# Performance work log

Measured on AMD Instinct MI355X. Metric: run time of the kernel, lower is better.

The kernel has to match this reference:

```python
import jax, jax.numpy as jnp
import numpy as np

N = 50000
E = 800000
IN_DIM = 128
HID = 128
OUT = 128
HEADS = 4
HD_HID = HID // HEADS   # 32
HD_OUT = OUT // HEADS   # 32
NEG_SLOPE = 0.2


def gat_layer(H, src, dst, W, a_src, a_dst, b, num_nodes):
    """Standard GAT layer with concatenated heads.
    H: [N, Fin]; W: [Fin, heads*hd]; a_src/a_dst: [heads, hd]; b: [heads*hd]."""
    heads, hd = a_src.shape
    h = (H @ W).reshape(num_nodes, heads, hd)            # [N, H, D]
    alpha_s = jnp.einsum('nhd,hd->nh', h, a_src)         # [N, H]
    alpha_d = jnp.einsum('nhd,hd->nh', h, a_dst)         # [N, H]
    logits = alpha_s[src] + alpha_d[dst]                 # [E, H]
    logits = jax.nn.leaky_relu(logits, NEG_SLOPE)
    # segment softmax over incoming edges of each destination node
    seg_max = jax.ops.segment_max(logits, dst, num_segments=num_nodes)
    seg_max = jnp.where(jnp.isfinite(seg_max), seg_max, 0.0)
    ex = jnp.exp(logits - seg_max[dst])                  # [E, H]
    denom = jax.ops.segment_sum(ex, dst, num_segments=num_nodes)  # [N, H]
    att = ex / jnp.maximum(denom, 1e-16)[dst]            # [E, H]
    msg = att[:, :, None] * h[src]                       # [E, H, D]
    out = jax.ops.segment_sum(msg, dst, num_segments=num_nodes)   # [N, H, D]
    return out.reshape(num_nodes, heads * hd) + b


def setup_inputs() -> dict:
    key = jax.random.key(0)
    ks = jax.random.split(key, 10)
    X_all = jax.random.normal(ks[0], (N, IN_DIM), dtype=jnp.float32)
    edge_index = jax.random.randint(ks[1], (2, E), 0, N, dtype=jnp.int64)
    s0 = 1.0 / np.sqrt(IN_DIM)
    s1 = 1.0 / np.sqrt(HID)
    W0 = jax.random.normal(ks[2], (IN_DIM, HEADS * HD_HID), dtype=jnp.float32) * s0
    a_src0 = jax.random.normal(ks[3], (HEADS, HD_HID), dtype=jnp.float32) * s1
    a_dst0 = jax.random.normal(ks[4], (HEADS, HD_HID), dtype=jnp.float32) * s1
    b0 = jnp.zeros((HEADS * HD_HID,), dtype=jnp.float32)
    W1 = jax.random.normal(ks[5], (HID, HEADS * HD_OUT), dtype=jnp.float32) * s1
    a_src1 = jax.random.normal(ks[6], (HEADS, HD_OUT), dtype=jnp.float32) * s1
    a_dst1 = jax.random.normal(ks[7], (HEADS, HD_OUT), dtype=jnp.float32) * s1
    b1 = jnp.zeros((HEADS * HD_OUT,), dtype=jnp.float32)
    return {"X_all": X_all, "edge_index": edge_index,
            "W0": W0, "a_src0": a_src0, "a_dst0": a_dst0, "b0": b0,
            "W1": W1, "a_src1": a_src1, "a_dst1": a_dst1, "b1": b1}


def reference(X_all, edge_index, W0, a_src0, a_dst0, b0, W1, a_src1, a_dst1, b1):
    src, dst = edge_index[0], edge_index[1]
    num_nodes = X_all.shape[0]
    # layer 1 + ELU (dropout is identity in eval mode)
    H = gat_layer(X_all, src, dst, W0, a_src0, a_dst0, b0, num_nodes)
    H = jax.nn.elu(H)
    # layer 2 + ELU
    H = gat_layer(H, src, dst, W1, a_src1, a_dst1, b1, num_nodes)
    H = jax.nn.elu(H)
    return H
```

## Files before the change

kernel.cpp:

```cpp
#include <hip/hip_runtime.h>
#include <math.h>
#include <float.h>

#define NNODES 50000
#define NEDGES 800000

#define KB    196
#define NPB   256
#define CAPB  4608
#define EPB   4096
#define NABLK ((NEDGES + EPB - 1) / EPB)

typedef __attribute__((ext_vector_type(4))) _Float16 half4;
typedef __attribute__((ext_vector_type(8))) _Float16 half8;
typedef __attribute__((ext_vector_type(4))) float f32x4;

__global__ __launch_bounds__(256) void bininit_kernel(int* __restrict__ bincur) {
    int t = threadIdx.x;
    if (t < KB) bincur[t] = t * CAPB;
}

__global__ __launch_bounds__(256) void binA_kernel(
    const int* __restrict__ src, const int* __restrict__ dst,
    int* __restrict__ bincur, unsigned* __restrict__ binned)
{
    __shared__ int lhist[KB];
    __shared__ int lstart[KB];
    __shared__ int lcur[KB];
    __shared__ int gbase[KB];
    __shared__ unsigned lbuf[EPB];
    __shared__ int wtot[4];

    int t = threadIdx.x;
    int e0 = blockIdx.x * EPB;
    int ecnt = NEDGES - e0; if (ecnt > EPB) ecnt = EPB;

    for (int b = t; b < KB; b += 256) lhist[b] = 0;
    __syncthreads();

    for (int idx = t; idx < ecnt; idx += 256)
        atomicAdd(&lhist[((unsigned)dst[e0 + idx]) >> 8], 1);
    __syncthreads();

    {
        int lane = t & 63, w = t >> 6;
        int v = (t < KB) ? lhist[t] : 0;
        int x = v;
#pragma unroll
        for (int off = 1; off < 64; off <<= 1) {
            int y = __shfl_up(x, off, 64);
            if (lane >= off) x += y;
        }
        if (lane == 63) wtot[w] = x;
        __syncthreads();
        int wpre = 0;
#pragma unroll
        for (int j = 0; j < 4; ++j) if (j < w) wpre += wtot[j];
        int ex = wpre + x - v;
        if (t < KB) { lstart[t] = ex; lcur[t] = ex; }
    }
    __syncthreads();

    if (t < KB) {
        int c = lhist[t];
        gbase[t] = c ? atomicAdd(&bincur[t], c) : 0;
    }
    __syncthreads();

    for (int idx = t; idx < ecnt; idx += 256) {
        unsigned d = (unsigned)dst[e0 + idx];
        unsigned s = (unsigned)src[e0 + idx];
        int pos = atomicAdd(&lcur[d >> 8], 1);
        lbuf[pos] = (d << 16) | s;
    }
    __syncthreads();

    for (int idx = t; idx < ecnt; idx += 256) {
        unsigned p = lbuf[idx];
        int b = p >> 24;
        binned[gbase[b] + (idx - lstart[b])] = p;
    }
}

__global__ __launch_bounds__(256) void binB_kernel(
    const unsigned* __restrict__ binned, const int* __restrict__ bincur,
    int* __restrict__ csr_src, int2* __restrict__ node_info)
{
    __shared__ int lhist[NPB];
    __shared__ int lcur[NPB];
    __shared__ int wtot[4];
    int k = blockIdx.x;
    int t = threadIdx.x;
    int base = k * CAPB;
    int cnt = bincur[k] - base;

    lhist[t] = 0;
    __syncthreads();

    for (int i = t; i < cnt; i += 256)
        atomicAdd(&lhist[(binned[base + i] >> 16) & 0xFF], 1);
    __syncthreads();

    int lane = t & 63, w = t >> 6;
    int v = lhist[t];
    int x = v;
#pragma unroll
    for (int off = 1; off < 64; off <<= 1) {
        int y = __shfl_up(x, off, 64);
        if (lane >= off) x += y;
    }
    if (lane == 63) wtot[w] = x;
    __syncthreads();
    int wpre = 0;
#pragma unroll
    for (int j = 0; j < 4; ++j) if (j < w) wpre += wtot[j];
    int ex = wpre + x - v;
    lcur[t] = ex;
    int node = k * NPB + t;
    if (node < NNODES) node_info[node] = make_int2(base + ex, v);
    __syncthreads();

    for (int i = t; i < cnt; i += 256) {
        unsigned p = binned[base + i];
        int ln = (p >> 16) & 0xFF;
        int pos = atomicAdd(&lcur[ln], 1);
        csr_src[base + pos] = (int)(p & 0xFFFFu);
    }
}

__global__ __launch_bounds__(256) void prep_kernel(
    const float* __restrict__ X, const float* __restrict__ W0,
    const float* __restrict__ W1, _Float16* __restrict__ X16,
    _Float16* __restrict__ W0t, _Float16* __restrict__ W1t)
{
    int i = blockIdx.x * 256 + threadIdx.x;
    int stride = gridDim.x * 256;
    const int nx4 = NNODES * 128 / 4;
    for (int idx = i; idx < nx4; idx += stride) {
        float4 v = ((const float4*)X)[idx];
        half4 h = {(_Float16)v.x, (_Float16)v.y, (_Float16)v.z, (_Float16)v.w};
        ((half4*)X16)[idx] = h;
    }
    for (int idx = i; idx < 128 * 128; idx += stride) {
        int cc = idx >> 7, k = idx & 127;
        W0t[idx] = (_Float16)W0[k * 128 + cc];
        W1t[idx] = (_Float16)W1[k * 128 + cc];
    }
}

#define GP 136
__global__ __launch_bounds__(256) void gemm_mfma_kernel(
    const _Float16* __restrict__ A, const _Float16* __restrict__ Wt,
    const float* __restrict__ avs, const float* __restrict__ avd,
    _Float16* __restrict__ Hh, float* __restrict__ alpha_s,
    float* __restrict__ alpha_d, int nrows)
{
    __shared__ _Float16 Xs[64 * GP];
    __shared__ _Float16 Ws[128 * GP];

    int t = threadIdx.x;
    int brow = blockIdx.x * 64;

    {
        int r = t >> 2, q = t & 3;
        int grow = brow + r;
        half8 v0 = {}, v1 = {}, v2 = {}, v3 = {};
        if (grow < nrows) {
            const half8* p = (const half8*)(A + (size_t)grow * 128 + q * 32);
            v0 = p[0]; v1 = p[1]; v2 = p[2]; v3 = p[3];
        }
        _Float16* d = Xs + r * GP + q * 32;
        *(half8*)(d + 0)  = v0; *(half8*)(d + 8)  = v1;
        *(half8*)(d + 16) = v2; *(half8*)(d + 24) = v3;
    }
    {
        int wr = t >> 1, wh = t & 1;
        const half8* p = (const half8*)(Wt + wr * 128 + wh * 64);
        _Float16* d = Ws + wr * GP + wh * 64;
#pragma unroll
        for (int j = 0; j < 8; ++j) *(half8*)(d + j * 8) = p[j];
    }
    __syncthreads();

    int wv = t >> 6, l = t & 63;
    int lrow = l & 15;
    int lk8  = (l >> 4) * 8;

    f32x4 acc[8];
#pragma unroll
    for (int n = 0; n < 8; ++n) acc[n] = (f32x4){0.f, 0.f, 0.f, 0.f};

    const _Float16* xbase = Xs + (wv * 16 + lrow) * GP + lk8;
#pragma unroll
    for (int kk = 0; kk < 4; ++kk) {
        half8 a = *(const half8*)(xbase + kk * 32);
#pragma unroll
        for (int n = 0; n < 8; ++n) {
            half8 bf = *(const half8*)(Ws + (n * 16 + lrow) * GP + kk * 32 + lk8);
            acc[n] = __builtin_amdgcn_mfma_f32_16x16x32_f16(a, bf, acc[n], 0, 0, 0);
        }
    }

    int c = lrow;
    int g = l >> 4;
#pragma unroll
    for (int n = 0; n < 8; ++n) {
#pragma unroll
        for (int r = 0; r < 4; ++r) {
            int row = brow + wv * 16 + g * 4 + r;
            if (row < nrows)
                Hh[(size_t)row * 128 + n * 16 + c] = (_Float16)acc[n][r];
        }
    }
#pragma unroll
    for (int hd = 0; hd < 4; ++hd) {
        float as0 = avs[hd * 32 + c], as1 = avs[hd * 32 + 16 + c];
        float ad0 = avd[hd * 32 + c], ad1 = avd[hd * 32 + 16 + c];
#pragma unroll
        for (int r = 0; r < 4; ++r) {
            float ps = acc[2 * hd][r] * as0 + acc[2 * hd + 1][r] * as1;
            float pd = acc[2 * hd][r] * ad0 + acc[2 * hd + 1][r] * ad1;
            ps += __shfl_xor(ps, 1); ps += __shfl_xor(ps, 2);
            ps += __shfl_xor(ps, 4); ps += __shfl_xor(ps, 8);
            pd += __shfl_xor(pd, 1); pd += __shfl_xor(pd, 2);
            pd += __shfl_xor(pd, 4); pd += __shfl_xor(pd, 8);
            if (c == 0) {
                int row = brow + wv * 16 + g * 4 + r;
                if (row < nrows) {
                    alpha_s[row * 4 + hd] = ps;
                    alpha_d[row * 4 + hd] = pd;
                }
            }
        }
    }
}

template <bool F16OUT>
__global__ __launch_bounds__(256) void att_gather_kernel(
    const int* __restrict__ csr_src, const int2* __restrict__ node_info,
    const float* __restrict__ alpha_s, const float* __restrict__ alpha_d,
    const _Float16* __restrict__ hbuf, const float* __restrict__ b,
    float* __restrict__ out32, _Float16* __restrict__ out16)
{
    int node = blockIdx.x * 4 + (threadIdx.x >> 6);
    if (node >= NNODES) return;
    int lane = threadIdx.x & 63;
    int half = lane >> 5;
    int q    = lane & 31;
    int f    = q * 4;
    int hh   = q >> 3;
    int2 bi = node_info[node];
    int beg = bi.x, end = bi.x + bi.y;
    float ad = alpha_d[node * 4 + hh];

    float4 a4 = make_float4(0.f, 0.f, 0.f, 0.f);
    float den = 0.f;
    int i = beg + half;
    for (; i + 6 < end; i += 8) {
        int s0 = csr_src[i];
        int s1 = csr_src[i + 2];
        int s2 = csr_src[i + 4];
        int s3 = csr_src[i + 6];
        float l0 = alpha_s[s0 * 4 + hh] + ad;
        float l1 = alpha_s[s1 * 4 + hh] + ad;
        float l2 = alpha_s[s2 * 4 + hh] + ad;
        float l3 = alpha_s[s3 * 4 + hh] + ad;
        half4 h0 = *(const half4*)(hbuf + (size_t)s0 * 128 + f);
        half4 h1 = *(const half4*)(hbuf + (size_t)s1 * 128 + f);
        half4 h2 = *(const half4*)(hbuf + (size_t)s2 * 128 + f);
        half4 h3 = *(const half4*)(hbuf + (size_t)s3 * 128 + f);
        l0 = (l0 >= 0.f) ? l0 : 0.2f * l0;
        l1 = (l1 >= 0.f) ? l1 : 0.2f * l1;
        l2 = (l2 >= 0.f) ? l2 : 0.2f * l2;
        l3 = (l3 >= 0.f) ? l3 : 0.2f * l3;
        float e0 = __expf(l0);
        float e1 = __expf(l1);
        float e2 = __expf(l2);
        float e3 = __expf(l3);
        den += (e0 + e1) + (e2 + e3);
        a4.x = fmaf(e0, (float)h0[0], a4.x); a4.y = fmaf(e0, (float)h0[1], a4.y);
        a4.z = fmaf(e0, (float)h0[2], a4.z); a4.w = fmaf(e0, (float)h0[3], a4.w);
        a4.x = fmaf(e1, (float)h1[0], a4.x); a4.y = fmaf(e1, (float)h1[1], a4.y);
        a4.z = fmaf(e1, (float)h1[2], a4.z); a4.w = fmaf(e1, (float)h1[3], a4.w);
        a4.x = fmaf(e2, (float)h2[0], a4.x); a4.y = fmaf(e2, (float)h2[1], a4.y);
        a4.z = fmaf(e2, (float)h2[2], a4.z); a4.w = fmaf(e2, (float)h2[3], a4.w);
        a4.x = fmaf(e3, (float)h3[0], a4.x); a4.y = fmaf(e3, (float)h3[1], a4.y);
        a4.z = fmaf(e3, (float)h3[2], a4.z); a4.w = fmaf(e3, (float)h3[3], a4.w);
    }
    for (; i < end; i += 2) {
        int s0 = csr_src[i];
        float l0 = alpha_s[s0 * 4 + hh] + ad;
        l0 = (l0 >= 0.f) ? l0 : 0.2f * l0;
        float e0 = __expf(l0);
        half4 h0 = *(const half4*)(hbuf + (size_t)s0 * 128 + f);
        den += e0;
        a4.x = fmaf(e0, (float)h0[0], a4.x); a4.y = fmaf(e0, (float)h0[1], a4.y);
        a4.z = fmaf(e0, (float)h0[2], a4.z); a4.w = fmaf(e0, (float)h0[3], a4.w);
    }

    a4.x += __shfl_xor(a4.x, 32);
    a4.y += __shfl_xor(a4.y, 32);
    a4.z += __shfl_xor(a4.z, 32);
    a4.w += __shfl_xor(a4.w, 32);
    den  += __shfl_xor(den, 32);

    if (half == 0) {
        float rd = 1.f / fmaxf(den, 1e-16f);
        float4 bv = *(const float4*)(b + f);
        float x0 = a4.x * rd + bv.x;
        float x1 = a4.y * rd + bv.y;
        float x2 = a4.z * rd + bv.z;
        float x3 = a4.w * rd + bv.w;
        x0 = (x0 > 0.f) ? x0 : expm1f(x0);
        x1 = (x1 > 0.f) ? x1 : expm1f(x1);
        x2 = (x2 > 0.f) ? x2 : expm1f(x2);
        x3 = (x3 > 0.f) ? x3 : expm1f(x3);
        if (F16OUT) {
            half4 hv = {(_Float16)x0, (_Float16)x1, (_Float16)x2, (_Float16)x3};
            *(half4*)(out16 + (size_t)node * 128 + f) = hv;
        } else {
            *(float4*)(out32 + (size_t)node * 128 + f) = make_float4(x0, x1, x2, x3);
        }
    }
}

extern "C" void kernel_launch(void* const* d_in, const int* in_sizes, int n_in,
                              void* d_out, int out_size, void* d_ws, size_t ws_size,
                              hipStream_t stream) {
    const float* X    = (const float*)d_in[0];
    const int*   ei   = (const int*)d_in[1];
    const float* W0   = (const float*)d_in[2];
    const float* as0  = (const float*)d_in[3];
    const float* ad0  = (const float*)d_in[4];
    const float* b0   = (const float*)d_in[5];
    const float* W1   = (const float*)d_in[6];
    const float* as1  = (const float*)d_in[7];
    const float* ad1  = (const float*)d_in[8];
    const float* b1   = (const float*)d_in[9];

    const int* srcp = ei;
    const int* dstp = ei + NEDGES;

    _Float16* X16  = (_Float16*)d_ws;
    _Float16* h16  = X16 + 6400000;
    _Float16* ho16 = h16 + 6400000;
    _Float16* W0t  = ho16 + 6400000;
    _Float16* W1t  = W0t + 16384;
    float* as_ = (float*)(W1t + 16384);
    float* ad_ = as_ + 200000;
    unsigned* binned = (unsigned*)(ad_ + 200000);
    int*  csr_src   = (int*)(binned + (KB + 1) * CAPB);
    int2* node_info = (int2*)(csr_src + KB * CAPB);
    int*  bincur    = (int*)(node_info + NNODES);

    bininit_kernel<<<1, 256, 0, stream>>>(bincur);
    binA_kernel<<<NABLK, 256, 0, stream>>>(srcp, dstp, bincur, binned);
    binB_kernel<<<KB, 256, 0, stream>>>(binned, bincur, csr_src, node_info);

    prep_kernel<<<2048, 256, 0, stream>>>(X, W0, W1, X16, W0t, W1t);

    const int NODE_BLOCKS = (NNODES + 3) / 4;
    const int GEMM_BLOCKS = (NNODES + 63) / 64;

    gemm_mfma_kernel<<<GEMM_BLOCKS, 256, 0, stream>>>(
        X16, W0t, as0, ad0, h16, as_, ad_, NNODES);
    att_gather_kernel<true><<<NODE_BLOCKS, 256, 0, stream>>>(
        csr_src, node_info, as_, ad_, h16, b0, nullptr, ho16);

    gemm_mfma_kernel<<<GEMM_BLOCKS, 256, 0, stream>>>(
        ho16, W1t, as1, ad1, h16, as_, ad_, NNODES);
    att_gather_kernel<false><<<NODE_BLOCKS, 256, 0, stream>>>(
        csr_src, node_info, as_, ad_, h16, b1, (float*)d_out, nullptr);
}
```

Baseline: 160.2 us.

## Fuse fp32-to-fp16 input conversion into GEMM and widen gather to half8 lanes

The separate X-to-fp16 conversion pass is removed. The first GEMM now reads fp32 X directly and converts it while staging into shared memory, which saves a full write and re-read of a 12.8 MB fp16 copy. The attention gather is reorganised so each node's wave has 16 lanes each covering 8 features with half8 loads, and 4 edge groups run in parallel, reduced with two shuffles. This raises edge-level parallelism and vector width per load, but loop unrolling drops from 4 edges to 2 per iteration and the epilogue adds an extra shuffle stage.

```diff
diff --git a/kernel.cpp b/kernel.cpp
--- a/kernel.cpp
+++ b/kernel.cpp
@@ -128,20 +128,12 @@
     }
 }
 
-__global__ __launch_bounds__(256) void prep_kernel(
-    const float* __restrict__ X, const float* __restrict__ W0,
-    const float* __restrict__ W1, _Float16* __restrict__ X16,
+__global__ __launch_bounds__(256) void prepw_kernel(
+    const float* __restrict__ W0, const float* __restrict__ W1,
     _Float16* __restrict__ W0t, _Float16* __restrict__ W1t)
 {
-    int i = blockIdx.x * 256 + threadIdx.x;
-    int stride = gridDim.x * 256;
-    const int nx4 = NNODES * 128 / 4;
-    for (int idx = i; idx < nx4; idx += stride) {
-        float4 v = ((const float4*)X)[idx];
-        half4 h = {(_Float16)v.x, (_Float16)v.y, (_Float16)v.z, (_Float16)v.w};
-        ((half4*)X16)[idx] = h;
-    }
-    for (int idx = i; idx < 128 * 128; idx += stride) {
+    int idx = blockIdx.x * 256 + threadIdx.x;
+    if (idx < 128 * 128) {
         int cc = idx >> 7, k = idx & 127;
         W0t[idx] = (_Float16)W0[k * 128 + cc];
         W1t[idx] = (_Float16)W1[k * 128 + cc];
@@ -149,8 +141,9 @@
 }
 
 #define GP 136
+template <bool F32IN>
 __global__ __launch_bounds__(256) void gemm_mfma_kernel(
-    const _Float16* __restrict__ A, const _Float16* __restrict__ Wt,
+    const void* __restrict__ Ain, const _Float16* __restrict__ Wt,
     const float* __restrict__ avs, const float* __restrict__ avd,
     _Float16* __restrict__ Hh, float* __restrict__ alpha_s,
     float* __restrict__ alpha_d, int nrows)
@@ -164,14 +157,33 @@
     {
         int r = t >> 2, q = t & 3;
         int grow = brow + r;
-        half8 v0 = {}, v1 = {}, v2 = {}, v3 = {};
-        if (grow < nrows) {
-            const half8* p = (const half8*)(A + (size_t)grow * 128 + q * 32);
-            v0 = p[0]; v1 = p[1]; v2 = p[2]; v3 = p[3];
-        }
         _Float16* d = Xs + r * GP + q * 32;
-        *(half8*)(d + 0)  = v0; *(half8*)(d + 8)  = v1;
-        *(half8*)(d + 16) = v2; *(half8*)(d + 24) = v3;
+        if (F32IN) {
+            const float* A32 = (const float*)Ain;
+            float4 v[8];
+#pragma unroll
+            for (int j = 0; j < 8; ++j) v[j] = make_float4(0, 0, 0, 0);
+            if (grow < nrows) {
+                const float4* p = (const float4*)(A32 + (size_t)grow * 128 + q * 32);
+#pragma unroll
+                for (int j = 0; j < 8; ++j) v[j] = p[j];
+            }
+#pragma unroll
+            for (int j = 0; j < 8; ++j) {
+                half4 h = {(_Float16)v[j].x, (_Float16)v[j].y,
+                           (_Float16)v[j].z, (_Float16)v[j].w};
+                *(half4*)(d + j * 4) = h;
+            }
+        } else {
+            const _Float16* A16 = (const _Float16*)Ain;
+            half8 v0 = {}, v1 = {}, v2 = {}, v3 = {};
+            if (grow < nrows) {
+                const half8* p = (const half8*)(A16 + (size_t)grow * 128 + q * 32);
+                v0 = p[0]; v1 = p[1]; v2 = p[2]; v3 = p[3];
+            }
+            *(half8*)(d + 0)  = v0; *(half8*)(d + 8)  = v1;
+            *(half8*)(d + 16) = v2; *(half8*)(d + 24) = v3;
+        }
     }
     {
         int wr = t >> 1, wh = t & 1;
@@ -245,81 +257,74 @@
     int node = blockIdx.x * 4 + (threadIdx.x >> 6);
     if (node >= NNODES) return;
     int lane = threadIdx.x & 63;
-    int half = lane >> 5;
-    int q    = lane & 31;
-    int f    = q * 4;
-    int hh   = q >> 3;
+    int p  = lane >> 4;
+    int ft = lane & 15;
+    int f  = ft * 8;
+    int hh = ft >> 2;
     int2 bi = node_info[node];
     int beg = bi.x, end = bi.x + bi.y;
     float ad = alpha_d[node * 4 + hh];
 
-    float4 a4 = make_float4(0.f, 0.f, 0.f, 0.f);
+    float acc[8] = {0.f, 0.f, 0.f, 0.f, 0.f, 0.f, 0.f, 0.f};
     float den = 0.f;
-    int i = beg + half;
-    for (; i + 6 < end; i += 8) {
+    int i = beg + p;
+    for (; i + 4 < end; i += 8) {
         int s0 = csr_src[i];
-        int s1 = csr_src[i + 2];
-        int s2 = csr_src[i + 4];
-        int s3 = csr_src[i + 6];
+        int s1 = csr_src[i + 4];
         float l0 = alpha_s[s0 * 4 + hh] + ad;
         float l1 = alpha_s[s1 * 4 + hh] + ad;
-        float l2 = alpha_s[s2 * 4 + hh] + ad;
-        float l3 = alpha_s[s3 * 4 + hh] + ad;
-        half4 h0 = *(const half4*)(hbuf + (size_t)s0 * 128 + f);
-        half4 h1 = *(const half4*)(hbuf + (size_t)s1 * 128 + f);
-        half4 h2 = *(const half4*)(hbuf + (size_t)s2 * 128 + f);
-        half4 h3 = *(const half4*)(hbuf + (size_t)s3 * 128 + f);
-        l0 = (l0 >= 0.f) ? l0 : 0.2f * l0;
-        l1 = (l1 >= 0.f) ? l1 : 0.2f * l1;
-        l2 = (l2 >= 0.f) ? l2 : 0.2f * l2;
-        l3 = (l3 >= 0.f) ? l3 : 0.2f * l3;
+        half8 h0 = *(const half8*)(hbuf + (size_t)s0 * 128 + f);
+        half8 h1 = *(const half8*)(hbuf + (size_t)s1 * 128 + f);
+        l0 = fmaxf(l0, 0.2f * l0);
+        l1 = fmaxf(l1, 0.2f * l1);
         float e0 = __expf(l0);
         float e1 = __expf(l1);
-        float e2 = __expf(l2);
-        float e3 = __expf(l3);
-        den += (e0 + e1) + (e2 + e3);
-        a4.x = fmaf(e0, (float)h0[0], a4.x); a4.y = fmaf(e0, (float)h0[1], a4.y);
-        a4.z = fmaf(e0, (float)h0[2], a4.z); a4.w = fmaf(e0, (float)h0[3], a4.w);
-        a4.x = fmaf(e1, (float)h1[0], a4.x); a4.y = fmaf(e1, (float)h1[1], a4.y);
-        a4.z = fmaf(e1, (float)h1[2], a4.z); a4.w = fmaf(e1, (float)h1[3], a4.w);
-        a4.x = fmaf(e2, (float)h2[0], a4.x); a4.y = fmaf(e2, (float)h2[1], a4.y);
-        a4.z = fmaf(e2, (float)h2[2], a4.z); a4.w = fmaf(e2, (float)h2[3], a4.w);
-        a4.x = fmaf(e3, (float)h3[0], a4.x); a4.y = fmaf(e3, (float)h3[1], a4.y);
-        a4.z = fmaf(e3, (float)h3[2], a4.z); a4.w = fmaf(e3, (float)h3[3], a4.w);
-    }
-    for (; i < end; i += 2) {
+        den += e0 + e1;
+#pragma unroll
+        for (int j = 0; j < 8; ++j) acc[j] = fmaf(e0, (float)h0[j], acc[j]);
+#pragma unroll
+        for (int j = 0; j < 8; ++j) acc[j] = fmaf(e1, (float)h1[j], acc[j]);
+    }
+    for (; i < end; i += 4) {
         int s0 = csr_src[i];
         float l0 = alpha_s[s0 * 4 + hh] + ad;
-        l0 = (l0 >= 0.f) ? l0 : 0.2f * l0;
+        half8 h0 = *(const half8*)(hbuf + (size_t)s0 * 128 + f);
+        l0 = fmaxf(l0, 0.2f * l0);
         float e0 = __expf(l0);
-        half4 h0 = *(const half4*)(hbuf + (size_t)s0 * 128 + f);
         den += e0;
-        a4.x = fmaf(e0, (float)h0[0], a4.x); a4.y = fmaf(e0, (float)h0[1], a4.y);
-        a4.z = fmaf(e0, (float)h0[2], a4.z); a4.w = fmaf(e0, (float)h0[3], a4.w);
-    }
-
-    a4.x += __shfl_xor(a4.x, 32);
-    a4.y += __shfl_xor(a4.y, 32);
-    a4.z += __shfl_xor(a4.z, 32);
-    a4.w += __shfl_xor(a4.w, 32);
-    den  += __shfl_xor(den, 32);
-
-    if (half == 0) {
+#pragma unroll
+        for (int j = 0; j < 8; ++j) acc[j] = fmaf(e0, (float)h0[j], acc[j]);
+    }
+
+#pragma unroll
+    for (int j = 0; j < 8; ++j) {
+        acc[j] += __shfl_xor(acc[j], 16);
+        acc[j] += __shfl_xor(acc[j], 32);
+    }
+    den += __shfl_xor(den, 16);
+    den += __shfl_xor(den, 32);
+
+    if (p == 0) {
         float rd = 1.f / fmaxf(den, 1e-16f);
-        float4 bv = *(const float4*)(b + f);
-        float x0 = a4.x * rd + bv.x;
-        float x1 = a4.y * rd + bv.y;
-        float x2 = a4.z * rd + bv.z;
-        float x3 = a4.w * rd + bv.w;
-        x0 = (x0 > 0.f) ? x0 : expm1f(x0);
-        x1 = (x1 > 0.f) ? x1 : expm1f(x1);
-        x2 = (x2 > 0.f) ? x2 : expm1f(x2);
-        x3 = (x3 > 0.f) ? x3 : expm1f(x3);
+        float4 bv0 = *(const float4*)(b + f);
+        float4 bv1 = *(const float4*)(b + f + 4);
+        float x[8];
+        x[0] = acc[0] * rd + bv0.x; x[1] = acc[1] * rd + bv0.y;
+        x[2] = acc[2] * rd + bv0.z; x[3] = acc[3] * rd + bv0.w;
+        x[4] = acc[4] * rd + bv1.x; x[5] = acc[5] * rd + bv1.y;
+        x[6] = acc[6] * rd + bv1.z; x[7] = acc[7] * rd + bv1.w;
+#pragma unroll
+        for (int j = 0; j < 8; ++j) x[j] = (x[j] > 0.f) ? x[j] : expm1f(x[j]);
         if (F16OUT) {
-            half4 hv = {(_Float16)x0, (_Float16)x1, (_Float16)x2, (_Float16)x3};
-            *(half4*)(out16 + (size_t)node * 128 + f) = hv;
+            half8 hv;
+#pragma unroll
+            for (int j = 0; j < 8; ++j) hv[j] = (_Float16)x[j];
+            *(half8*)(out16 + (size_t)node * 128 + f) = hv;
         } else {
-            *(float4*)(out32 + (size_t)node * 128 + f) = make_float4(x0, x1, x2, x3);
+            *(float4*)(out32 + (size_t)node * 128 + f) =
+                make_float4(x[0], x[1], x[2], x[3]);
+            *(float4*)(out32 + (size_t)node * 128 + f + 4) =
+                make_float4(x[4], x[5], x[6], x[7]);
         }
     }
 }
@@ -341,8 +346,7 @@
     const int* srcp = ei;
     const int* dstp = ei + NEDGES;
 
-    _Float16* X16  = (_Float16*)d_ws;
-    _Float16* h16  = X16 + 6400000;
+    _Float16* h16  = (_Float16*)d_ws;
     _Float16* ho16 = h16 + 6400000;
     _Float16* W0t  = ho16 + 6400000;
     _Float16* W1t  = W0t + 16384;
@@ -357,17 +361,17 @@
     binA_kernel<<<NABLK, 256, 0, stream>>>(srcp, dstp, bincur, binned);
     binB_kernel<<<KB, 256, 0, stream>>>(binned, bincur, csr_src, node_info);
 
-    prep_kernel<<<2048, 256, 0, stream>>>(X, W0, W1, X16, W0t, W1t);
+    prepw_kernel<<<64, 256, 0, stream>>>(W0, W1, W0t, W1t);
 
     const int NODE_BLOCKS = (NNODES + 3) / 4;
     const int GEMM_BLOCKS = (NNODES + 63) / 64;
 
-    gemm_mfma_kernel<<<GEMM_BLOCKS, 256, 0, stream>>>(
-        X16, W0t, as0, ad0, h16, as_, ad_, NNODES);
+    gemm_mfma_kernel<true><<<GEMM_BLOCKS, 256, 0, stream>>>(
+        X, W0t, as0, ad0, h16, as_, ad_, NNODES);
     att_gather_kernel<true><<<NODE_BLOCKS, 256, 0, stream>>>(
         csr_src, node_info, as_, ad_, h16, b0, nullptr, ho16);
 
-    gemm_mfma_kernel<<<GEMM_BLOCKS, 256, 0, stream>>>(
+    gemm_mfma_kernel<false><<<GEMM_BLOCKS, 256, 0, stream>>>(
         ho16, W1t, as1, ad1, h16, as_, ad_, NNODES);
     att_gather_kernel<false><<<NODE_BLOCKS, 256, 0, stream>>>(
         csr_src, node_info, as_, ad_, h16, b1, (float*)d_out, nullptr);
```

Result: faster. 156.5 us (-2.3%).
